# Performance work log

Hardware: AMD Instinct MI355X
Metric: run time of the kernel (lower is better)

## Reference

```python
import jax, jax.numpy as jnp
import numpy as np

NEG_SLOPE = 0.2  # PyG GATConv default leaky_relu slope


def _gat_layer(x, src, dst, n_nodes, W, a_src, a_dst, b, heads, out_ch):
    # x: [N, Fin] -> h: [N, H, C]
    h = (x @ W).reshape(n_nodes, heads, out_ch)
    alpha_s = jnp.einsum('nhc,hc->nh', h, a_src)  # [N, H]
    alpha_d = jnp.einsum('nhc,hc->nh', h, a_dst)  # [N, H]
    e = jax.nn.leaky_relu(alpha_s[src] + alpha_d[dst], NEG_SLOPE)  # [E, H]
    # segment softmax over edges grouped by destination node
    m = jax.ops.segment_max(e, dst, num_segments=n_nodes)          # [N, H]
    e = jnp.exp(e - m[dst])
    denom = jax.ops.segment_sum(e, dst, num_segments=n_nodes)      # [N, H]
    alpha = e / denom[dst]                                          # self-loops guarantee denom > 0
    msg = alpha[:, :, None] * h[src]                                # [E, H, C]
    out = jax.ops.segment_sum(msg, dst, num_segments=n_nodes)      # [N, H, C]
    return out.reshape(n_nodes, heads * out_ch) + b


def reference(x, edge_index, batch, W1, a_src1, a_dst1, b1, W2, a_src2, a_dst2, b2, fc_w, fc_b):
    n_nodes = x.shape[0]
    heads = a_src1.shape[0]
    # PyG GATConv adds self-loops by default
    loops = jnp.arange(n_nodes, dtype=edge_index.dtype)
    src = jnp.concatenate([edge_index[0], loops])
    dst = jnp.concatenate([edge_index[1], loops])

    h = _gat_layer(x, src, dst, n_nodes, W1, a_src1, a_dst1, b1, heads, 64)
    h = jax.nn.relu(h)  # dropout is identity in eval mode
    h = _gat_layer(h, src, dst, n_nodes, W2, a_src2, a_dst2, b2, heads, 16)
    h = jax.nn.relu(h)

    n_graphs = 64
    sums = jax.ops.segment_sum(h, batch, num_segments=n_graphs)                    # [G, 64]
    counts = jax.ops.segment_sum(jnp.ones((n_nodes,), h.dtype), batch, num_segments=n_graphs)
    pooled = sums / jnp.maximum(counts, 1.0)[:, None]                              # global_mean_pool
    return pooled @ fc_w + fc_b


def setup_inputs() -> dict:
    key = jax.random.key(0)
    ks = jax.random.split(key, 12)
    N, E, F_in, G = 50000, 800000, 128, 64
    H = 4
    x = jax.random.normal(ks[0], (N, F_in), jnp.float32)
    edge_index = jax.random.randint(ks[1], (2, E), 0, N, jnp.int32)
    batch = jnp.sort(jax.random.randint(ks[2], (N,), 0, G, jnp.int32))
    s1 = 1.0 / np.sqrt(F_in)
    s2 = 1.0 / np.sqrt(H * 64)
    s3 = 1.0 / np.sqrt(H * 16)
    return {
        'x': x,
        'edge_index': edge_index,
        'batch': batch,
        'W1': jax.random.normal(ks[3], (F_in, H * 64), jnp.float32) * s1,
        'a_src1': jax.random.normal(ks[4], (H, 64), jnp.float32) * s1,
        'a_dst1': jax.random.normal(ks[5], (H, 64), jnp.float32) * s1,
        'b1': jnp.zeros((H * 64,), jnp.float32),
        'W2': jax.random.normal(ks[6], (H * 64, H * 16), jnp.float32) * s2,
        'a_src2': jax.random.normal(ks[7], (H, 16), jnp.float32) * s2,
        'a_dst2': jax.random.normal(ks[8], (H, 16), jnp.float32) * s2,
        'b2': jnp.zeros((H * 16,), jnp.float32),
        'fc_w': jax.random.normal(ks[9], (H * 16, 32), jnp.float32) * s3,
        'fc_b': jnp.zeros((32,), jnp.float32),
    }
```

## Files before the change

### kernel.cpp

```cpp
#include <hip/hip_runtime.h>
#include <hip/hip_bf16.h>
#include <hip/hip_fp16.h>
#include <math.h>

#define HEADS 4
#define CAP 64

typedef _Float16 half8_t __attribute__((ext_vector_type(8)));
typedef float float4_t __attribute__((ext_vector_type(4)));


__global__ __launch_bounds__(256) void prep_k(int* cnt, unsigned short* slots, int N, int NB,
                                              const float* __restrict__ W1, _Float16* __restrict__ W1T,
                                              const float* __restrict__ W2, _Float16* __restrict__ W2T) {
    int bx = blockIdx.x;
    if (bx < NB) {
        int i = bx * 256 + threadIdx.x;
        if (i < N) {
            cnt[i] = 1;
            slots[(size_t)i * CAP] = (unsigned short)i;
        }
    } else if (bx < NB + 128) {
        int k = bx - NB;
        int n = threadIdx.x;
        W1T[n * 128 + k] = (_Float16)W1[k * 256 + n];
    } else {
        int n = bx - NB - 128;
        int k = threadIdx.x;
        W2T[n * 256 + k] = (_Float16)W2[k * 64 + n];
    }
}


__global__ __launch_bounds__(256) void fused_scatter_gemm1_k(
    const int* __restrict__ src, const int* __restrict__ dst,
    int* __restrict__ cnt, unsigned short* __restrict__ slots, int E, int SB,
    const float* __restrict__ A,
    const _Float16* __restrict__ BT,
    __half* __restrict__ hout,
    const float* __restrict__ avs,
    const float* __restrict__ avd,
    float* __restrict__ os,
    float* __restrict__ od, int M) {
    __shared__ _Float16 lds[4 * 16 * 72];

    if ((int)blockIdx.x < SB) {
        int T = SB * 256;
        int t0 = blockIdx.x * 256 + threadIdx.x;
        int d[8], s[8];
        #pragma unroll
        for (int k = 0; k < 8; k++) {
            int i = t0 + k * T;
            if (i < E) { d[k] = dst[i]; s[k] = src[i]; }
            else d[k] = -1;
        }
        int p[8];
        #pragma unroll
        for (int k = 0; k < 8; k++) {
            if (d[k] >= 0) p[k] = atomicAdd(&cnt[d[k]], 1);
        }
        #pragma unroll
        for (int k = 0; k < 8; k++) {
            if (d[k] >= 0 && p[k] < CAP)
                slots[(size_t)d[k] * CAP + p[k]] = (unsigned short)s[k];
        }
        return;
    }

    int bx = blockIdx.x - SB;
    int wave = threadIdx.x >> 6;
    int lane = threadIdx.x & 63;
    int q = lane >> 4;
    int c16 = lane & 15;
    int row0 = bx * 64 + wave * 16;

    half8_t a[4];
    int ar = row0 + c16;
    bool avalid = (ar < M);
    const float* ap = A + (size_t)ar * 128;
    #pragma unroll
    for (int ks = 0; ks < 4; ks++) {
        if (avalid) {
            float4 f0 = *(const float4*)(ap + ks * 32 + q * 8);
            float4 f1 = *(const float4*)(ap + ks * 32 + q * 8 + 4);
            half8_t h;
            h[0] = (_Float16)f0.x; h[1] = (_Float16)f0.y;
            h[2] = (_Float16)f0.z; h[3] = (_Float16)f0.w;
            h[4] = (_Float16)f1.x; h[5] = (_Float16)f1.y;
            h[6] = (_Float16)f1.z; h[7] = (_Float16)f1.w;
            a[ks] = h;
        } else {
            a[ks] = (half8_t)(_Float16)0.0f;
        }
    }

    float4_t acc[16];
    #pragma unroll
    for (int ct = 0; ct < 16; ct++) acc[ct] = (float4_t)0.f;

    #pragma unroll
    for (int ks = 0; ks < 4; ks++) {
        #pragma unroll
        for (int ct = 0; ct < 16; ct++) {
            half8_t b = *(const half8_t*)(BT + (size_t)(ct * 16 + c16) * 128 + ks * 32 + q * 8);
            acc[ct] = __builtin_amdgcn_mfma_f32_16x16x32_f16(a[ks], b, acc[ct], 0, 0, 0);
        }
    }

    float psh[4][4] = {}, pdh[4][4] = {};
    #pragma unroll
    for (int ct = 0; ct < 16; ct++) {
        int h = ct >> 2;
        int cih = (ct & 3) * 16 + c16;
        float as_v = avs[h * 64 + cih];
        float ad_v = avd[h * 64 + cih];
        #pragma unroll
        for (int r = 0; r < 4; r++) {
            psh[h][r] = fmaf(acc[ct][r], as_v, psh[h][r]);
            pdh[h][r] = fmaf(acc[ct][r], ad_v, pdh[h][r]);
        }
    }
    #pragma unroll
    for (int h = 0; h < 4; h++) {
        #pragma unroll
        for (int r = 0; r < 4; r++) {
            #pragma unroll
            for (int o = 8; o >= 1; o >>= 1) {
                psh[h][r] += __shfl_down(psh[h][r], o, 16);
                pdh[h][r] += __shfl_down(pdh[h][r], o, 16);
            }
        }
    }
    if (c16 == 0) {
        #pragma unroll
        for (int r = 0; r < 4; r++) {
            int gr = row0 + q * 4 + r;
            if (gr < M) {
                #pragma unroll
                for (int h = 0; h < 4; h++) {
                    os[(size_t)gr * HEADS + h] = psh[h][r];
                    od[(size_t)gr * HEADS + h] = pdh[h][r];
                }
            }
        }
    }

    _Float16* wl = lds + wave * (16 * 72);
    #pragma unroll
    for (int chunk = 0; chunk < 4; chunk++) {
        #pragma unroll
        for (int c4 = 0; c4 < 4; c4++) {
            int ct = chunk * 4 + c4;
            #pragma unroll
            for (int r = 0; r < 4; r++) {
                wl[(q * 4 + r) * 72 + c4 * 16 + c16] = (_Float16)acc[ct][r];
            }
        }
        __syncthreads();
        #pragma unroll
        for (int pass = 0; pass < 2; pass++) {
            int idx8 = pass * 64 + lane;
            int row = idx8 >> 3;
            int col8 = idx8 & 7;
            int gr = row0 + row;
            if (gr < M) {
                *(half8_t*)(hout + (size_t)gr * 256 + chunk * 64 + col8 * 8) =
                    *(const half8_t*)(wl + row * 72 + col8 * 8);
            }
        }
        __syncthreads();
    }
}


__global__ __launch_bounds__(256) void mfma_gemm2_k(
    const _Float16* __restrict__ Ah,
    const _Float16* __restrict__ BT,
    __half* __restrict__ hout,
    const float* __restrict__ avs,
    const float* __restrict__ avd,
    float* __restrict__ os,
    float* __restrict__ od, int M) {
    __shared__ _Float16 lds[4 * 16 * 64];
    int wave = threadIdx.x >> 6;
    int lane = threadIdx.x & 63;
    int q = lane >> 4;
    int c16 = lane & 15;
    int row0 = blockIdx.x * 64 + wave * 16;

    half8_t a[8];
    int ar = row0 + c16;
    bool avalid = (ar < M);
    const _Float16* ap = Ah + (size_t)ar * 256;
    #pragma unroll
    for (int ks = 0; ks < 8; ks++) {
        if (avalid) a[ks] = *(const half8_t*)(ap + ks * 32 + q * 8);
        else        a[ks] = (half8_t)(_Float16)0.0f;
    }

    float4_t acc[4];
    #pragma unroll
    for (int ct = 0; ct < 4; ct++) acc[ct] = (float4_t)0.f;

    #pragma unroll
    for (int ks = 0; ks < 8; ks++) {
        #pragma unroll
        for (int ct = 0; ct < 4; ct++) {
            half8_t b = *(const half8_t*)(BT + (size_t)(ct * 16 + c16) * 256 + ks * 32 + q * 8);
            acc[ct] = __builtin_amdgcn_mfma_f32_16x16x32_f16(a[ks], b, acc[ct], 0, 0, 0);
        }
    }

    float ps[4][4], pd[4][4];
    #pragma unroll
    for (int ct = 0; ct < 4; ct++) {
        float as_v = avs[ct * 16 + c16];
        float ad_v = avd[ct * 16 + c16];
        #pragma unroll
        for (int r = 0; r < 4; r++) {
            ps[ct][r] = acc[ct][r] * as_v;
            pd[ct][r] = acc[ct][r] * ad_v;
            #pragma unroll
            for (int o = 8; o >= 1; o >>= 1) {
                ps[ct][r] += __shfl_down(ps[ct][r], o, 16);
                pd[ct][r] += __shfl_down(pd[ct][r], o, 16);
            }
        }
    }
    if (c16 == 0) {
        #pragma unroll
        for (int r = 0; r < 4; r++) {
            int gr = row0 + q * 4 + r;
            if (gr < M) {
                #pragma unroll
                for (int ct = 0; ct < 4; ct++) {
                    os[(size_t)gr * HEADS + ct] = ps[ct][r];
                    od[(size_t)gr * HEADS + ct] = pd[ct][r];
                }
            }
        }
    }

    _Float16* wl = lds + wave * (16 * 64);
    #pragma unroll
    for (int ct = 0; ct < 4; ct++) {
        #pragma unroll
        for (int r = 0; r < 4; r++) {
            wl[(q * 4 + r) * 64 + ct * 16 + c16] = (_Float16)acc[ct][r];
        }
    }
    __syncthreads();
    #pragma unroll
    for (int pass = 0; pass < 2; pass++) {
        int idx8 = pass * 64 + lane;
        int row = idx8 >> 3;
        int col8 = idx8 & 7;
        int gr = row0 + row;
        if (gr < M) {
            *(half8_t*)(hout + (size_t)gr * 64 + col8 * 8) =
                *(const half8_t*)(wl + row * 64 + col8 * 8);
        }
    }
}


__global__ __launch_bounds__(256) void gat_agg64_f16_k(
    const __half* __restrict__ hsrc,
    const float* __restrict__ as,
    const float* __restrict__ ad,
    const int* __restrict__ cnt,
    const unsigned short* __restrict__ slots,
    const float* __restrict__ bias,
    __half* __restrict__ outh,
    int N) {
    int node = blockIdx.x * 4 + (threadIdx.x >> 6);
    if (node >= N) return;
    int l = threadIdx.x & 63;
    int h = l >> 4;
    int je = l & 15;
    int hb = h << 4;
    int deg = min(cnt[node], CAP);
    const unsigned short* sp = slots + (size_t)node * CAP;
    float adh = ad[(size_t)node * HEADS + h];
    float4 bv = *(const float4*)(bias + l * 4);

    int sv[4];
    float ev[4];
    #pragma unroll
    for (int k = 0; k < 4; k++) {
        int j = k * 16 + je;
        sv[k] = (j < deg) ? (int)sp[j] : 0;
    }
    #pragma unroll
    for (int k = 0; k < 4; k++) {
        int j = k * 16 + je;
        if (j < deg) {
            float a = as[(size_t)sv[k] * HEADS + h] + adh;
            ev[k] = (a > 0.f) ? a : 0.2f * a;
        } else {
            ev[k] = -INFINITY;
        }
    }
    float m = fmaxf(fmaxf(ev[0], ev[1]), fmaxf(ev[2], ev[3]));
    #pragma unroll
    for (int o = 8; o >= 1; o >>= 1) m = fmaxf(m, __shfl_xor(m, o));
    float pv[4];
    float den = 0.f;
    #pragma unroll
    for (int k = 0; k < 4; k++) {
        pv[k] = (k * 16 + je < deg) ? __expf(ev[k] - m) : 0.f;
        den += pv[k];
    }
    #pragma unroll
    for (int o = 8; o >= 1; o >>= 1) den += __shfl_xor(den, o);

    float4 acc = make_float4(0.f, 0.f, 0.f, 0.f);
    #pragma unroll
    for (int k = 0; k < 4; k++) {
        int base = k * 16;
        if (base >= deg) break;
        int cl = min(16, deg - base);
        #pragma unroll
        for (int half = 0; half < 2; half++) {
            int j0 = half * 8;
            if (j0 >= cl) break;
            float pj[8]; int sj[8];
            #pragma unroll
            for (int jj = 0; jj < 8; jj++) {
                pj[jj] = __shfl(pv[k], hb + j0 + jj);
                sj[jj] = __shfl(sv[k], hb + j0 + jj);
            }
            uint2 rv[8];
            #pragma unroll
            for (int jj = 0; jj < 8; jj++) {
                if (j0 + jj < cl) rv[jj] = *(const uint2*)(hsrc + (size_t)sj[jj] * 256 + l * 4);
            }
            #pragma unroll
            for (int jj = 0; jj < 8; jj++) {
                if (j0 + jj < cl) {
                    float2 a0 = __half22float2(*(__half2*)&rv[jj].x);
                    float2 b0 = __half22float2(*(__half2*)&rv[jj].y);
                    acc.x = fmaf(pj[jj], a0.x, acc.x); acc.y = fmaf(pj[jj], a0.y, acc.y);
                    acc.z = fmaf(pj[jj], b0.x, acc.z); acc.w = fmaf(pj[jj], b0.y, acc.w);
                }
            }
        }
    }

    float inv = 1.f / den;
    float rx = fmaxf(fmaf(acc.x, inv, bv.x), 0.f);
    float ry = fmaxf(fmaf(acc.y, inv, bv.y), 0.f);
    float rz = fmaxf(fmaf(acc.z, inv, bv.z), 0.f);
    float rw = fmaxf(fmaf(acc.w, inv, bv.w), 0.f);
    __half2* op = (__half2*)(outh + (size_t)node * 256 + l * 4);
    op[0] = __floats2half2_rn(rx, ry);
    op[1] = __floats2half2_rn(rz, rw);
}


__global__ __launch_bounds__(256) void gat_agg16_f16_k(
    const __half* __restrict__ hsrc,
    const float* __restrict__ as,
    const float* __restrict__ ad,
    const int* __restrict__ cnt,
    const unsigned short* __restrict__ slots,
    const float* __restrict__ bias,
    float* __restrict__ out, int N) {
    int node = blockIdx.x * 4 + (threadIdx.x >> 6);
    if (node >= N) return;
    int l = threadIdx.x & 63;
    int ha = l >> 4;
    int je = l & 15;
    int q = l & 15;
    int hh = q >> 2;
    int eg = l >> 4;
    int deg = min(cnt[node], CAP);
    const unsigned short* sp = slots + (size_t)node * CAP;
    float adh = ad[(size_t)node * HEADS + ha];
    float m = -INFINITY, den = 0.f;
    float4 acc = make_float4(0.f, 0.f, 0.f, 0.f);
    for (int base = 0; base < deg; base += 16) {
        int cl = min(16, deg - base);
        int s = 0;
        float e = -INFINITY;
        if (je < cl) {
            s = sp[base + je];
            float a = as[(size_t)s * HEADS + ha] + adh;
            e = (a > 0.f) ? a : 0.2f * a;
        }
        float cmax = e;
        #pragma unroll
        for (int o = 8; o >= 1; o >>= 1) cmax = fmaxf(cmax, __shfl_xor(cmax, o));
        float m_new = fmaxf(m, cmax);
        float p = (je < cl) ? __expf(e - m_new) : 0.f;
        float sum = p;
        #pragma unroll
        for (int o = 8; o >= 1; o >>= 1) sum += __shfl_xor(sum, o);
        float sc = __expf(m - m_new);
        den = den * sc + sum;
        m = m_new;
        float sch = __shfl(sc, hh << 4);
        acc.x *= sch; acc.y *= sch; acc.z *= sch; acc.w *= sch;

        int jbase = eg * 4;
        float pj[4]; int sj[4]; bool vj[4];
        #pragma unroll
        for (int jj = 0; jj < 4; jj++) {
            int j = jbase + jj;
            int jc = min(j, cl - 1);
            pj[jj] = __shfl(p, (hh << 4) + jc);
            sj[jj] = __shfl(s, (hh << 4) + jc);
            vj[jj] = (j < cl);
        }
        uint2 rv[4];
        #pragma unroll
        for (int jj = 0; jj < 4; jj++) {
            if (vj[jj]) rv[jj] = *(const uint2*)(hsrc + (size_t)sj[jj] * 64 + q * 4);
        }
        #pragma unroll
        for (int jj = 0; jj < 4; jj++) {
            if (vj[jj]) {
                float2 f0 = __half22float2(*(__half2*)&rv[jj].x);
                float2 f1 = __half22float2(*(__half2*)&rv[jj].y);
                acc.x = fmaf(pj[jj], f0.x, acc.x); acc.y = fmaf(pj[jj], f0.y, acc.y);
                acc.z = fmaf(pj[jj], f1.x, acc.z); acc.w = fmaf(pj[jj], f1.y, acc.w);
            }
        }
    }
    acc.x += __shfl_xor(acc.x, 16); acc.y += __shfl_xor(acc.y, 16);
    acc.z += __shfl_xor(acc.z, 16); acc.w += __shfl_xor(acc.w, 16);
    acc.x += __shfl_xor(acc.x, 32); acc.y += __shfl_xor(acc.y, 32);
    acc.z += __shfl_xor(acc.z, 32); acc.w += __shfl_xor(acc.w, 32);
    float denh = __shfl(den, hh << 4);
    if (eg == 0) {
        float inv = 1.f / denh;
        float4 bv = *(const float4*)(bias + q * 4);
        float4 r;
        r.x = fmaxf(fmaf(acc.x, inv, bv.x), 0.f);
        r.y = fmaxf(fmaf(acc.y, inv, bv.y), 0.f);
        r.z = fmaxf(fmaf(acc.z, inv, bv.z), 0.f);
        r.w = fmaxf(fmaf(acc.w, inv, bv.w), 0.f);
        *(float4*)(out + (size_t)node * 64 + q * 4) = r;
    }
}


__global__ __launch_bounds__(256) void bounds_zero_k(const int* __restrict__ batch, int N,
                                                     int* __restrict__ bstart,
                                                     float* __restrict__ sums) {
    int t = threadIdx.x;
    if (t <= 64) {
        int lo = 0, hi = N;
        while (lo < hi) {
            int mid = (lo + hi) >> 1;
            if (batch[mid] < t) lo = mid + 1; else hi = mid;
        }
        bstart[t] = lo;
    }
    for (int i = t; i < 64 * 64; i += 256) sums[i] = 0.f;
}

__global__ __launch_bounds__(256) void pool_sum_k(const float* __restrict__ g2,
                                                  const int* __restrict__ batch,
                                                  float* __restrict__ sums, int N) {
    int c = threadIdx.x & 63;
    int r = threadIdx.x >> 6;
    int base = blockIdx.x * 256;
    int lim = min(base + 256, N);
    float acc = 0.f;
    int cur = -1;
    for (int n = base + r; n < lim; n += 4) {
        int g = batch[n];
        if (g != cur) {
            if (cur >= 0) atomicAdd(&sums[cur * 64 + c], acc);
            acc = 0.f;
            cur = g;
        }
        acc += g2[(size_t)n * 64 + c];
    }
    if (cur >= 0) atomicAdd(&sums[cur * 64 + c], acc);
}

__global__ void fc_k(const float* __restrict__ sums, const int* __restrict__ bstart,
                     const float* __restrict__ w, const float* __restrict__ b,
                     float* __restrict__ out) {
    int g = blockIdx.x, o = threadIdx.x;
    float cnt_ = (float)max(bstart[g + 1] - bstart[g], 1);
    float inv = 1.f / cnt_;
    float acc = b[o];
    for (int k = 0; k < 64; k++) acc = fmaf(sums[g * 64 + k] * inv, w[k * 32 + o], acc);
    out[g * 32 + o] = acc;
}


static inline size_t align_up(size_t x, size_t a) { return (x + a - 1) & ~(a - 1); }

extern "C" void kernel_launch(void* const* d_in, const int* in_sizes, int n_in,
                              void* d_out, int out_size, void* d_ws, size_t ws_size,
                              hipStream_t stream) {
    const float* x      = (const float*)d_in[0];
    const int*   ei     = (const int*)d_in[1];
    const int*   batch  = (const int*)d_in[2];
    const float* W1     = (const float*)d_in[3];
    const float* a_src1 = (const float*)d_in[4];
    const float* a_dst1 = (const float*)d_in[5];
    const float* b1     = (const float*)d_in[6];
    const float* W2     = (const float*)d_in[7];
    const float* a_src2 = (const float*)d_in[8];
    const float* a_dst2 = (const float*)d_in[9];
    const float* b2     = (const float*)d_in[10];
    const float* fc_w   = (const float*)d_in[11];
    const float* fc_b   = (const float*)d_in[12];
    float* out = (float*)d_out;

    const int N = in_sizes[2];
    const int E = in_sizes[1] / 2;
    const int F_in = in_sizes[0] / N;
    const int D1 = HEADS * 64;
    const int D2 = HEADS * 16;

    const int* src = ei;
    const int* dst = ei + E;

    char* w = (char*)d_ws;
    size_t off = 0;
    auto alloc = [&](size_t bytes) {
        size_t p = off;
        off = align_up(off + bytes, 256);
        return (void*)(w + p);
    };
    int* cnt    = (int*)alloc((size_t)N * 4);
    unsigned short* slots = (unsigned short*)alloc((size_t)N * CAP * 2);
    int* bstart = (int*)alloc(65 * 4);
    float* pooled = (float*)alloc(64 * 64 * 4);
    float* as1  = (float*)alloc((size_t)N * HEADS * 4);
    float* ad1  = (float*)alloc((size_t)N * HEADS * 4);
    float* as2  = (float*)alloc((size_t)N * HEADS * 4);
    float* ad2  = (float*)alloc((size_t)N * HEADS * 4);
    __half* h1h = (__half*)alloc((size_t)N * D1 * 2);
    __half* g1h = (__half*)alloc((size_t)N * D1 * 2);
    __half* h2h = (__half*)alloc((size_t)N * D2 * 2);
    float* g2   = (float*)alloc((size_t)N * D2 * 4);
    _Float16* w1t = (_Float16*)alloc((size_t)F_in * D1 * 2);
    _Float16* w2t = (_Float16*)alloc((size_t)D1 * D2 * 2);

    const int NB = (N + 255) / 256;
    prep_k<<<NB + 128 + 64, 256, 0, stream>>>(cnt, slots, N, NB, W1, w1t, W2, w2t);

    const int SB = (E + 2047) / 2048;
    const int GB = (N + 63) / 64;
    fused_scatter_gemm1_k<<<SB + GB, 256, 0, stream>>>(
        src, dst, cnt, slots, E, SB,
        x, w1t, h1h, a_src1, a_dst1, as1, ad1, N);

    gat_agg64_f16_k<<<(N + 3) / 4, 256, 0, stream>>>(h1h, as1, ad1, cnt, slots, b1, g1h, N);

    mfma_gemm2_k<<<(N + 63) / 64, 256, 0, stream>>>((const _Float16*)g1h, w2t, h2h,
                                                    a_src2, a_dst2, as2, ad2, N);
    gat_agg16_f16_k<<<(N + 3) / 4, 256, 0, stream>>>(h2h, as2, ad2, cnt, slots, b2, g2, N);

    bounds_zero_k<<<1, 256, 0, stream>>>(batch, N, bstart, pooled);
    pool_sum_k<<<(N + 255) / 256, 256, 0, stream>>>(g2, batch, pooled, N);
    fc_k<<<64, 32, 0, stream>>>(pooled, bstart, fc_w, fc_b, out);
}
```

Baseline: 314.0 us.

## Replace global atomic edge scatter with chunked LDS byte-counter histogram and scan

Replaces the global-memory atomicAdd per edge on per-node counters with a two-pass scheme. Each of 128 edge chunks first builds a packed 8-bit per-node count histogram in LDS. A tiled column scan then turns those into per-chunk offsets, and a second pass places sources using LDS atomics. The bounds/zero kernel is also folded into prep_k. This aims to cut global atomic contention, but it adds a kernel launch, a 6.4MB count matrix and an extra read of dst. It also relies on 8-bit counters not overflowing: any carry out of a packed byte corrupts the neighbouring node's count, so high-degree nodes are a correctness risk.

```diff
diff --git a/kernel.cpp b/kernel.cpp
--- a/kernel.cpp
+++ b/kernel.cpp
@@ -5,36 +5,112 @@
 
 #define HEADS 4
 #define CAP 64
+#define NC 128
 
 typedef _Float16 half8_t __attribute__((ext_vector_type(8)));
 typedef float float4_t __attribute__((ext_vector_type(4)));
 
 
-__global__ __launch_bounds__(256) void prep_k(int* cnt, unsigned short* slots, int N, int NB,
+__global__ __launch_bounds__(256) void prep_k(unsigned short* slots, int N, int NB,
                                               const float* __restrict__ W1, _Float16* __restrict__ W1T,
-                                              const float* __restrict__ W2, _Float16* __restrict__ W2T) {
+                                              const float* __restrict__ W2, _Float16* __restrict__ W2T,
+                                              const int* __restrict__ dst, int E,
+                                              unsigned char* __restrict__ cnts8, int NS,
+                                              const int* __restrict__ batch,
+                                              int* __restrict__ bstart, float* __restrict__ sums) {
+    __shared__ unsigned int sh[12544];
     int bx = blockIdx.x;
-    if (bx < NB) {
-        int i = bx * 256 + threadIdx.x;
-        if (i < N) {
-            cnt[i] = 1;
-            slots[(size_t)i * CAP] = (unsigned short)i;
-        }
-    } else if (bx < NB + 128) {
-        int k = bx - NB;
+    if (bx < NC) {
+        int c = bx;
+        int nwt = NS >> 2;
+        for (int i = threadIdx.x; i < nwt; i += 256) sh[i] = 0u;
+        __syncthreads();
+        int epc = (E + NC - 1) / NC;
+        int lo = c * epc, hi = min(lo + epc, E);
+        for (int i = lo + threadIdx.x; i < hi; i += 256) {
+            int d = dst[i];
+            atomicAdd(&sh[d >> 2], 1u << ((d & 3) * 8));
+        }
+        __syncthreads();
+        unsigned int* row32 = (unsigned int*)(cnts8 + (size_t)c * NS);
+        for (int i = threadIdx.x; i < nwt; i += 256) row32[i] = sh[i];
+    } else if (bx < NC + NB) {
+        int i = (bx - NC) * 256 + threadIdx.x;
+        if (i < N) slots[(size_t)i * CAP] = (unsigned short)i;
+    } else if (bx < NC + NB + 128) {
+        int k = bx - NC - NB;
         int n = threadIdx.x;
         W1T[n * 128 + k] = (_Float16)W1[k * 256 + n];
-    } else {
-        int n = bx - NB - 128;
+    } else if (bx < NC + NB + 192) {
+        int n = bx - NC - NB - 128;
         int k = threadIdx.x;
         W2T[n * 256 + k] = (_Float16)W2[k * 64 + n];
-    }
-}
-
-
-__global__ __launch_bounds__(256) void fused_scatter_gemm1_k(
-    const int* __restrict__ src, const int* __restrict__ dst,
-    int* __restrict__ cnt, unsigned short* __restrict__ slots, int E, int SB,
+    } else {
+        int t = threadIdx.x;
+        if (t <= 64) {
+            int lo = 0, hi = N;
+            while (lo < hi) {
+                int mid = (lo + hi) >> 1;
+                if (batch[mid] < t) lo = mid + 1; else hi = mid;
+            }
+            bstart[t] = lo;
+        }
+        for (int i = t; i < 64 * 64; i += 256) sums[i] = 0.f;
+    }
+}
+
+
+__global__ __launch_bounds__(256) void scan_tile_k(unsigned char* __restrict__ cnts8,
+                                                   int NS, int N, int* __restrict__ cnt) {
+    __shared__ unsigned int tile[NC * 128];
+    int nwt = NS >> 2;
+    int wb = blockIdx.x * 128;
+    const unsigned int* g = (const unsigned int*)cnts8;
+    int rowstride = nwt;
+
+    for (int idx = threadIdx.x; idx < NC * 128; idx += 256) {
+        int c = idx >> 7;
+        int w = idx & 127;
+        int gw = wb + w;
+        if (gw < nwt) tile[c * 128 + w] = g[(size_t)c * rowstride + gw];
+    }
+    __syncthreads();
+
+    if (threadIdx.x < 128) {
+        int w = threadIdx.x;
+        int gw = wb + w;
+        if (gw < nwt) {
+            unsigned int a = 0x01010101u;
+            #pragma unroll 8
+            for (int c = 0; c < NC; c++) {
+                unsigned int v = tile[c * 128 + w];
+                tile[c * 128 + w] = a;
+                a += v;
+            }
+            int n0 = gw * 4;
+            #pragma unroll
+            for (int b = 0; b < 4; b++) {
+                int n = n0 + b;
+                if (n < N) cnt[n] = (int)((a >> (b * 8)) & 255u);
+            }
+        }
+    }
+    __syncthreads();
+
+    unsigned int* gm = (unsigned int*)cnts8;
+    for (int idx = threadIdx.x; idx < NC * 128; idx += 256) {
+        int c = idx >> 7;
+        int w = idx & 127;
+        int gw = wb + w;
+        if (gw < nwt) gm[(size_t)c * rowstride + gw] = tile[c * 128 + w];
+    }
+}
+
+
+__global__ __launch_bounds__(256) void fused_place_gemm1_k(
+    const int* __restrict__ src, const int* __restrict__ dst, int E,
+    unsigned char* __restrict__ offs8, int NS,
+    unsigned short* __restrict__ slots,
     const float* __restrict__ A,
     const _Float16* __restrict__ BT,
     __half* __restrict__ hout,
@@ -42,32 +118,28 @@
     const float* __restrict__ avd,
     float* __restrict__ os,
     float* __restrict__ od, int M) {
-    __shared__ _Float16 lds[4 * 16 * 72];
-
-    if ((int)blockIdx.x < SB) {
-        int T = SB * 256;
-        int t0 = blockIdx.x * 256 + threadIdx.x;
-        int d[8], s[8];
-        #pragma unroll
-        for (int k = 0; k < 8; k++) {
-            int i = t0 + k * T;
-            if (i < E) { d[k] = dst[i]; s[k] = src[i]; }
-            else d[k] = -1;
-        }
-        int p[8];
-        #pragma unroll
-        for (int k = 0; k < 8; k++) {
-            if (d[k] >= 0) p[k] = atomicAdd(&cnt[d[k]], 1);
-        }
-        #pragma unroll
-        for (int k = 0; k < 8; k++) {
-            if (d[k] >= 0 && p[k] < CAP)
-                slots[(size_t)d[k] * CAP + p[k]] = (unsigned short)s[k];
+    __shared__ unsigned int shmem[12544];
+
+    if ((int)blockIdx.x < NC) {
+        int c = blockIdx.x;
+        int nwt = NS >> 2;
+        const unsigned int* row = (const unsigned int*)(offs8 + (size_t)c * NS);
+        for (int i = threadIdx.x; i < nwt; i += 256) shmem[i] = row[i];
+        __syncthreads();
+        int epc = (E + NC - 1) / NC;
+        int lo = c * epc, hi = min(lo + epc, E);
+        for (int i = lo + threadIdx.x; i < hi; i += 256) {
+            int d = dst[i];
+            int s = src[i];
+            unsigned int old = atomicAdd(&shmem[d >> 2], 1u << ((d & 3) * 8));
+            int pos = (int)((old >> ((d & 3) * 8)) & 255u);
+            if (pos < CAP) slots[(size_t)d * CAP + pos] = (unsigned short)s;
         }
         return;
     }
 
-    int bx = blockIdx.x - SB;
+    _Float16* lds = (_Float16*)shmem;
+    int bx = blockIdx.x - NC;
     int wave = threadIdx.x >> 6;
     int lane = threadIdx.x & 63;
     int q = lane >> 4;
@@ -445,21 +517,6 @@
 }
 
 
-__global__ __launch_bounds__(256) void bounds_zero_k(const int* __restrict__ batch, int N,
-                                                     int* __restrict__ bstart,
-                                                     float* __restrict__ sums) {
-    int t = threadIdx.x;
-    if (t <= 64) {
-        int lo = 0, hi = N;
-        while (lo < hi) {
-            int mid = (lo + hi) >> 1;
-            if (batch[mid] < t) lo = mid + 1; else hi = mid;
-        }
-        bstart[t] = lo;
-    }
-    for (int i = t; i < 64 * 64; i += 256) sums[i] = 0.f;
-}
-
 __global__ __launch_bounds__(256) void pool_sum_k(const float* __restrict__ g2,
                                                   const int* __restrict__ batch,
                                                   float* __restrict__ sums, int N) {
@@ -518,6 +575,8 @@
     const int F_in = in_sizes[0] / N;
     const int D1 = HEADS * 64;
     const int D2 = HEADS * 16;
+    const int NS = (N + 3) & ~3;
+    const int nwt = NS >> 2;
 
     const int* src = ei;
     const int* dst = ei + E;
@@ -543,14 +602,17 @@
     float* g2   = (float*)alloc((size_t)N * D2 * 4);
     _Float16* w1t = (_Float16*)alloc((size_t)F_in * D1 * 2);
     _Float16* w2t = (_Float16*)alloc((size_t)D1 * D2 * 2);
+    unsigned char* cnts8 = (unsigned char*)alloc((size_t)NC * NS);
 
     const int NB = (N + 255) / 256;
-    prep_k<<<NB + 128 + 64, 256, 0, stream>>>(cnt, slots, N, NB, W1, w1t, W2, w2t);
-
-    const int SB = (E + 2047) / 2048;
+    prep_k<<<NC + NB + 192 + 1, 256, 0, stream>>>(slots, N, NB, W1, w1t, W2, w2t,
+                                                  dst, E, cnts8, NS, batch, bstart, pooled);
+
+    scan_tile_k<<<(nwt + 127) / 128, 256, 0, stream>>>(cnts8, NS, N, cnt);
+
     const int GB = (N + 63) / 64;
-    fused_scatter_gemm1_k<<<SB + GB, 256, 0, stream>>>(
-        src, dst, cnt, slots, E, SB,
+    fused_place_gemm1_k<<<NC + GB, 256, 0, stream>>>(
+        src, dst, E, cnts8, NS, slots,
         x, w1t, h1h, a_src1, a_dst1, as1, ad1, N);
 
     gat_agg64_f16_k<<<(N + 3) / 4, 256, 0, stream>>>(h1h, as1, ad1, cnt, slots, b1, g1h, N);
@@ -559,7 +621,6 @@
                                                     a_src2, a_dst2, as2, ad2, N);
     gat_agg16_f16_k<<<(N + 3) / 4, 256, 0, stream>>>(h2h, as2, ad2, cnt, slots, b2, g2, N);
 
-    bounds_zero_k<<<1, 256, 0, stream>>>(batch, N, bstart, pooled);
     pool_sum_k<<<(N + 255) / 256, 256, 0, stream>>>(g2, batch, pooled, N);
     fc_k<<<64, 32, 0, stream>>>(pooled, bstart, fc_w, fc_b, out);
 }
```

Result: no change. 315.7 us (+0.5%).

## Bucket edges by destination range in LDS counters and fuse pooling with FC

Applied to the files above, without the earlier changes.

The edge scatter no longer uses global atomics. Each of 256 blocks owns a contiguous range of destination nodes, scans the whole dst array, and keeps per-node counters in LDS, writing the final counts to global memory once at the end. The separate cnt/slots init, the bounds/zero kernel and the atomic pool_sum plus fc kernels are merged into prep_k and a single per-graph poolfc_k that reduces with no atomics. The trade is that every scatter block reads all of dst (about 256 times the dst traffic, mostly absorbed by L2), in exchange for removing contended global atomics and several kernel launches.

```diff
diff --git a/kernel.cpp b/kernel.cpp
--- a/kernel.cpp
+++ b/kernel.cpp
@@ -5,36 +5,42 @@
 
 #define HEADS 4
 #define CAP 64
+#define SBL 256
 
 typedef _Float16 half8_t __attribute__((ext_vector_type(8)));
 typedef float float4_t __attribute__((ext_vector_type(4)));
 
 
-__global__ __launch_bounds__(256) void prep_k(int* cnt, unsigned short* slots, int N, int NB,
-                                              const float* __restrict__ W1, _Float16* __restrict__ W1T,
-                                              const float* __restrict__ W2, _Float16* __restrict__ W2T) {
+__global__ __launch_bounds__(256) void prep_k(const float* __restrict__ W1, _Float16* __restrict__ W1T,
+                                              const float* __restrict__ W2, _Float16* __restrict__ W2T,
+                                              const int* __restrict__ batch, int N,
+                                              int* __restrict__ bstart) {
     int bx = blockIdx.x;
-    if (bx < NB) {
-        int i = bx * 256 + threadIdx.x;
-        if (i < N) {
-            cnt[i] = 1;
-            slots[(size_t)i * CAP] = (unsigned short)i;
-        }
-    } else if (bx < NB + 128) {
-        int k = bx - NB;
+    if (bx < 128) {
+        int k = bx;
         int n = threadIdx.x;
         W1T[n * 128 + k] = (_Float16)W1[k * 256 + n];
-    } else {
-        int n = bx - NB - 128;
+    } else if (bx < 192) {
+        int n = bx - 128;
         int k = threadIdx.x;
         W2T[n * 256 + k] = (_Float16)W2[k * 64 + n];
+    } else {
+        int t = threadIdx.x;
+        if (t <= 64) {
+            int lo = 0, hi = N;
+            while (lo < hi) {
+                int mid = (lo + hi) >> 1;
+                if (batch[mid] < t) lo = mid + 1; else hi = mid;
+            }
+            bstart[t] = lo;
+        }
     }
 }
 
 
 __global__ __launch_bounds__(256) void fused_scatter_gemm1_k(
-    const int* __restrict__ src, const int* __restrict__ dst,
-    int* __restrict__ cnt, unsigned short* __restrict__ slots, int E, int SB,
+    const int* __restrict__ src, const int* __restrict__ dst, int E,
+    int* __restrict__ cnt, unsigned short* __restrict__ slots, int Nn,
     const float* __restrict__ A,
     const _Float16* __restrict__ BT,
     __half* __restrict__ hout,
@@ -42,32 +48,71 @@
     const float* __restrict__ avd,
     float* __restrict__ os,
     float* __restrict__ od, int M) {
+    __shared__ int lc[512];
     __shared__ _Float16 lds[4 * 16 * 72];
 
-    if ((int)blockIdx.x < SB) {
-        int T = SB * 256;
-        int t0 = blockIdx.x * 256 + threadIdx.x;
-        int d[8], s[8];
-        #pragma unroll
-        for (int k = 0; k < 8; k++) {
-            int i = t0 + k * T;
-            if (i < E) { d[k] = dst[i]; s[k] = src[i]; }
-            else d[k] = -1;
-        }
-        int p[8];
-        #pragma unroll
-        for (int k = 0; k < 8; k++) {
-            if (d[k] >= 0) p[k] = atomicAdd(&cnt[d[k]], 1);
-        }
-        #pragma unroll
-        for (int k = 0; k < 8; k++) {
-            if (d[k] >= 0 && p[k] < CAP)
-                slots[(size_t)d[k] * CAP + p[k]] = (unsigned short)s[k];
-        }
+    if ((int)blockIdx.x < SBL) {
+        int b = blockIdx.x;
+        int NR = (Nn + SBL - 1) / SBL;
+        int lo = b * NR, hi = min(lo + NR, Nn);
+        int nloc = hi - lo;
+        int t = threadIdx.x;
+        for (int j = t; j < nloc; j += 256) {
+            lc[j] = 1;
+            slots[(size_t)(lo + j) * CAP] = (unsigned short)(lo + j);
+        }
+        __syncthreads();
+
+        const int4* dst4 = (const int4*)dst;
+        int nq = E >> 2;
+        int base = 0;
+        for (; base + 1024 <= nq; base += 1024) {
+            int4 v[4];
+            #pragma unroll
+            for (int k = 0; k < 4; k++) v[k] = dst4[base + t + k * 256];
+            #pragma unroll
+            for (int k = 0; k < 4; k++) {
+                int i0 = (base + t + k * 256) * 4;
+                int dd[4] = { v[k].x, v[k].y, v[k].z, v[k].w };
+                #pragma unroll
+                for (int e = 0; e < 4; e++) {
+                    int d = dd[e];
+                    if (d >= lo && d < hi) {
+                        int s = src[i0 + e];
+                        int pos = atomicAdd(&lc[d - lo], 1);
+                        if (pos < CAP) slots[(size_t)d * CAP + pos] = (unsigned short)s;
+                    }
+                }
+            }
+        }
+        for (int i4 = base + t; i4 < nq; i4 += 256) {
+            int4 v = dst4[i4];
+            int i0 = i4 * 4;
+            int dd[4] = { v.x, v.y, v.z, v.w };
+            #pragma unroll
+            for (int e = 0; e < 4; e++) {
+                int d = dd[e];
+                if (d >= lo && d < hi) {
+                    int s = src[i0 + e];
+                    int pos = atomicAdd(&lc[d - lo], 1);
+                    if (pos < CAP) slots[(size_t)d * CAP + pos] = (unsigned short)s;
+                }
+            }
+        }
+        for (int i = (nq << 2) + t; i < E; i += 256) {
+            int d = dst[i];
+            if (d >= lo && d < hi) {
+                int s = src[i];
+                int pos = atomicAdd(&lc[d - lo], 1);
+                if (pos < CAP) slots[(size_t)d * CAP + pos] = (unsigned short)s;
+            }
+        }
+        __syncthreads();
+        for (int j = t; j < nloc; j += 256) cnt[lo + j] = lc[j];
         return;
     }
 
-    int bx = blockIdx.x - SB;
+    int bx = blockIdx.x - SBL;
     int wave = threadIdx.x >> 6;
     int lane = threadIdx.x & 63;
     int q = lane >> 4;
@@ -445,51 +490,34 @@
 }
 
 
-__global__ __launch_bounds__(256) void bounds_zero_k(const int* __restrict__ batch, int N,
-                                                     int* __restrict__ bstart,
-                                                     float* __restrict__ sums) {
-    int t = threadIdx.x;
-    if (t <= 64) {
-        int lo = 0, hi = N;
-        while (lo < hi) {
-            int mid = (lo + hi) >> 1;
-            if (batch[mid] < t) lo = mid + 1; else hi = mid;
-        }
-        bstart[t] = lo;
-    }
-    for (int i = t; i < 64 * 64; i += 256) sums[i] = 0.f;
-}
-
-__global__ __launch_bounds__(256) void pool_sum_k(const float* __restrict__ g2,
-                                                  const int* __restrict__ batch,
-                                                  float* __restrict__ sums, int N) {
+__global__ __launch_bounds__(256) void poolfc_k(const float* __restrict__ g2,
+                                                const int* __restrict__ bstart,
+                                                const float* __restrict__ w,
+                                                const float* __restrict__ b,
+                                                float* __restrict__ out) {
+    __shared__ float red[4][64];
+    __shared__ float pooled[64];
+    int g = blockIdx.x;
+    int lo = bstart[g], hi = bstart[g + 1];
     int c = threadIdx.x & 63;
     int r = threadIdx.x >> 6;
-    int base = blockIdx.x * 256;
-    int lim = min(base + 256, N);
     float acc = 0.f;
-    int cur = -1;
-    for (int n = base + r; n < lim; n += 4) {
-        int g = batch[n];
-        if (g != cur) {
-            if (cur >= 0) atomicAdd(&sums[cur * 64 + c], acc);
-            acc = 0.f;
-            cur = g;
-        }
-        acc += g2[(size_t)n * 64 + c];
-    }
-    if (cur >= 0) atomicAdd(&sums[cur * 64 + c], acc);
-}
-
-__global__ void fc_k(const float* __restrict__ sums, const int* __restrict__ bstart,
-                     const float* __restrict__ w, const float* __restrict__ b,
-                     float* __restrict__ out) {
-    int g = blockIdx.x, o = threadIdx.x;
-    float cnt_ = (float)max(bstart[g + 1] - bstart[g], 1);
-    float inv = 1.f / cnt_;
-    float acc = b[o];
-    for (int k = 0; k < 64; k++) acc = fmaf(sums[g * 64 + k] * inv, w[k * 32 + o], acc);
-    out[g * 32 + o] = acc;
+    for (int n = lo + r; n < hi; n += 4) acc += g2[(size_t)n * 64 + c];
+    red[r][c] = acc;
+    __syncthreads();
+    if (threadIdx.x < 64) {
+        float inv = 1.f / (float)max(hi - lo, 1);
+        pooled[threadIdx.x] = (red[0][threadIdx.x] + red[1][threadIdx.x] +
+                               red[2][threadIdx.x] + red[3][threadIdx.x]) * inv;
+    }
+    __syncthreads();
+    if (threadIdx.x < 32) {
+        int o = threadIdx.x;
+        float a = b[o];
+        #pragma unroll 8
+        for (int k = 0; k < 64; k++) a = fmaf(pooled[k], w[k * 32 + o], a);
+        out[g * 32 + o] = a;
+    }
 }
 
 
@@ -532,7 +560,6 @@
     int* cnt    = (int*)alloc((size_t)N * 4);
     unsigned short* slots = (unsigned short*)alloc((size_t)N * CAP * 2);
     int* bstart = (int*)alloc(65 * 4);
-    float* pooled = (float*)alloc(64 * 64 * 4);
     float* as1  = (float*)alloc((size_t)N * HEADS * 4);
     float* ad1  = (float*)alloc((size_t)N * HEADS * 4);
     float* as2  = (float*)alloc((size_t)N * HEADS * 4);
@@ -544,13 +571,11 @@
     _Float16* w1t = (_Float16*)alloc((size_t)F_in * D1 * 2);
     _Float16* w2t = (_Float16*)alloc((size_t)D1 * D2 * 2);
 
-    const int NB = (N + 255) / 256;
-    prep_k<<<NB + 128 + 64, 256, 0, stream>>>(cnt, slots, N, NB, W1, w1t, W2, w2t);
-
-    const int SB = (E + 2047) / 2048;
+    prep_k<<<193, 256, 0, stream>>>(W1, w1t, W2, w2t, batch, N, bstart);
+
     const int GB = (N + 63) / 64;
-    fused_scatter_gemm1_k<<<SB + GB, 256, 0, stream>>>(
-        src, dst, cnt, slots, E, SB,
+    fused_scatter_gemm1_k<<<SBL + GB, 256, 0, stream>>>(
+        src, dst, E, cnt, slots, N,
         x, w1t, h1h, a_src1, a_dst1, as1, ad1, N);
 
     gat_agg64_f16_k<<<(N + 3) / 4, 256, 0, stream>>>(h1h, as1, ad1, cnt, slots, b1, g1h, N);
@@ -559,7 +584,5 @@
                                                     a_src2, a_dst2, as2, ad2, N);
     gat_agg16_f16_k<<<(N + 3) / 4, 256, 0, stream>>>(h2h, as2, ad2, cnt, slots, b2, g2, N);
 
-    bounds_zero_k<<<1, 256, 0, stream>>>(batch, N, bstart, pooled);
-    pool_sum_k<<<(N + 255) / 256, 256, 0, stream>>>(g2, batch, pooled, N);
-    fc_k<<<64, 32, 0, stream>>>(pooled, bstart, fc_w, fc_b, out);
-}
+    poolfc_k<<<64, 256, 0, stream>>>(g2, bstart, fc_w, fc_b, out);
+}
```

Result: slower. 554.9 us (+76.7%).

## Fuse pooling and FC into one kernel, fold bounds search into prep, widen gather batch

Applied to the files above, without the earlier changes.

Computes the graph boundary binary search inside the prep kernel, removing the standalone bounds/zero launch. Replaces the atomic pool_sum and fc kernels with a single per-graph kernel that reduces that graph's contiguous rows, averages them and applies the FC layer, saving two launches and the atomics. Also widens the layer-1 aggregation gather from batches of 8 to 16 neighbour loads in flight. The per-graph pool kernel runs only 64 blocks, each reading about 780 rows serially, so it may have less parallelism than the old atomic version.

```diff
diff --git a/kernel.cpp b/kernel.cpp
--- a/kernel.cpp
+++ b/kernel.cpp
@@ -12,7 +12,8 @@
 
 __global__ __launch_bounds__(256) void prep_k(int* cnt, unsigned short* slots, int N, int NB,
                                               const float* __restrict__ W1, _Float16* __restrict__ W1T,
-                                              const float* __restrict__ W2, _Float16* __restrict__ W2T) {
+                                              const float* __restrict__ W2, _Float16* __restrict__ W2T,
+                                              const int* __restrict__ batch, int* __restrict__ bstart) {
     int bx = blockIdx.x;
     if (bx < NB) {
         int i = bx * 256 + threadIdx.x;
@@ -24,10 +25,20 @@
         int k = bx - NB;
         int n = threadIdx.x;
         W1T[n * 128 + k] = (_Float16)W1[k * 256 + n];
-    } else {
+    } else if (bx < NB + 192) {
         int n = bx - NB - 128;
         int k = threadIdx.x;
         W2T[n * 256 + k] = (_Float16)W2[k * 64 + n];
+    } else {
+        int t = threadIdx.x;
+        if (t <= 64) {
+            int lo = 0, hi = N;
+            while (lo < hi) {
+                int mid = (lo + hi) >> 1;
+                if (batch[mid] < t) lo = mid + 1; else hi = mid;
+            }
+            bstart[t] = lo;
+        }
     }
 }
 
@@ -320,29 +331,22 @@
         int base = k * 16;
         if (base >= deg) break;
         int cl = min(16, deg - base);
-        #pragma unroll
-        for (int half = 0; half < 2; half++) {
-            int j0 = half * 8;
-            if (j0 >= cl) break;
-            float pj[8]; int sj[8];
-            #pragma unroll
-            for (int jj = 0; jj < 8; jj++) {
-                pj[jj] = __shfl(pv[k], hb + j0 + jj);
-                sj[jj] = __shfl(sv[k], hb + j0 + jj);
-            }
-            uint2 rv[8];
-            #pragma unroll
-            for (int jj = 0; jj < 8; jj++) {
-                if (j0 + jj < cl) rv[jj] = *(const uint2*)(hsrc + (size_t)sj[jj] * 256 + l * 4);
-            }
-            #pragma unroll
-            for (int jj = 0; jj < 8; jj++) {
-                if (j0 + jj < cl) {
-                    float2 a0 = __half22float2(*(__half2*)&rv[jj].x);
-                    float2 b0 = __half22float2(*(__half2*)&rv[jj].y);
-                    acc.x = fmaf(pj[jj], a0.x, acc.x); acc.y = fmaf(pj[jj], a0.y, acc.y);
-                    acc.z = fmaf(pj[jj], b0.x, acc.z); acc.w = fmaf(pj[jj], b0.y, acc.w);
-                }
+        int sj[16];
+        #pragma unroll
+        for (int jj = 0; jj < 16; jj++) sj[jj] = __shfl(sv[k], hb + jj);
+        uint2 rv[16];
+        #pragma unroll
+        for (int jj = 0; jj < 16; jj++) {
+            if (jj < cl) rv[jj] = *(const uint2*)(hsrc + (size_t)sj[jj] * 256 + l * 4);
+        }
+        #pragma unroll
+        for (int jj = 0; jj < 16; jj++) {
+            if (jj < cl) {
+                float pj = __shfl(pv[k], hb + jj);
+                float2 a0 = __half22float2(*(__half2*)&rv[jj].x);
+                float2 b0 = __half22float2(*(__half2*)&rv[jj].y);
+                acc.x = fmaf(pj, a0.x, acc.x); acc.y = fmaf(pj, a0.y, acc.y);
+                acc.z = fmaf(pj, b0.x, acc.z); acc.w = fmaf(pj, b0.y, acc.w);
             }
         }
     }
@@ -445,51 +449,34 @@
 }
 
 
-__global__ __launch_bounds__(256) void bounds_zero_k(const int* __restrict__ batch, int N,
-                                                     int* __restrict__ bstart,
-                                                     float* __restrict__ sums) {
-    int t = threadIdx.x;
-    if (t <= 64) {
-        int lo = 0, hi = N;
-        while (lo < hi) {
-            int mid = (lo + hi) >> 1;
-            if (batch[mid] < t) lo = mid + 1; else hi = mid;
-        }
-        bstart[t] = lo;
-    }
-    for (int i = t; i < 64 * 64; i += 256) sums[i] = 0.f;
-}
-
-__global__ __launch_bounds__(256) void pool_sum_k(const float* __restrict__ g2,
-                                                  const int* __restrict__ batch,
-                                                  float* __restrict__ sums, int N) {
+__global__ __launch_bounds__(256) void poolfc_k(const float* __restrict__ g2,
+                                                const int* __restrict__ bstart,
+                                                const float* __restrict__ w,
+                                                const float* __restrict__ b,
+                                                float* __restrict__ out) {
+    __shared__ float red[4][64];
+    __shared__ float pooled[64];
+    int g = blockIdx.x;
+    int lo = bstart[g], hi = bstart[g + 1];
     int c = threadIdx.x & 63;
     int r = threadIdx.x >> 6;
-    int base = blockIdx.x * 256;
-    int lim = min(base + 256, N);
     float acc = 0.f;
-    int cur = -1;
-    for (int n = base + r; n < lim; n += 4) {
-        int g = batch[n];
-        if (g != cur) {
-            if (cur >= 0) atomicAdd(&sums[cur * 64 + c], acc);
-            acc = 0.f;
-            cur = g;
-        }
-        acc += g2[(size_t)n * 64 + c];
-    }
-    if (cur >= 0) atomicAdd(&sums[cur * 64 + c], acc);
-}
-
-__global__ void fc_k(const float* __restrict__ sums, const int* __restrict__ bstart,
-                     const float* __restrict__ w, const float* __restrict__ b,
-                     float* __restrict__ out) {
-    int g = blockIdx.x, o = threadIdx.x;
-    float cnt_ = (float)max(bstart[g + 1] - bstart[g], 1);
-    float inv = 1.f / cnt_;
-    float acc = b[o];
-    for (int k = 0; k < 64; k++) acc = fmaf(sums[g * 64 + k] * inv, w[k * 32 + o], acc);
-    out[g * 32 + o] = acc;
+    for (int n = lo + r; n < hi; n += 4) acc += g2[(size_t)n * 64 + c];
+    red[r][c] = acc;
+    __syncthreads();
+    if (threadIdx.x < 64) {
+        float inv = 1.f / (float)max(hi - lo, 1);
+        pooled[threadIdx.x] = (red[0][threadIdx.x] + red[1][threadIdx.x] +
+                               red[2][threadIdx.x] + red[3][threadIdx.x]) * inv;
+    }
+    __syncthreads();
+    if (threadIdx.x < 32) {
+        int o = threadIdx.x;
+        float a = b[o];
+        #pragma unroll 8
+        for (int k = 0; k < 64; k++) a = fmaf(pooled[k], w[k * 32 + o], a);
+        out[g * 32 + o] = a;
+    }
 }
 
 
@@ -532,7 +519,6 @@
     int* cnt    = (int*)alloc((size_t)N * 4);
     unsigned short* slots = (unsigned short*)alloc((size_t)N * CAP * 2);
     int* bstart = (int*)alloc(65 * 4);
-    float* pooled = (float*)alloc(64 * 64 * 4);
     float* as1  = (float*)alloc((size_t)N * HEADS * 4);
     float* ad1  = (float*)alloc((size_t)N * HEADS * 4);
     float* as2  = (float*)alloc((size_t)N * HEADS * 4);
@@ -545,7 +531,8 @@
     _Float16* w2t = (_Float16*)alloc((size_t)D1 * D2 * 2);
 
     const int NB = (N + 255) / 256;
-    prep_k<<<NB + 128 + 64, 256, 0, stream>>>(cnt, slots, N, NB, W1, w1t, W2, w2t);
+    prep_k<<<NB + 192 + 1, 256, 0, stream>>>(cnt, slots, N, NB, W1, w1t, W2, w2t,
+                                             batch, bstart);
 
     const int SB = (E + 2047) / 2048;
     const int GB = (N + 63) / 64;
@@ -559,7 +546,5 @@
                                                     a_src2, a_dst2, as2, ad2, N);
     gat_agg16_f16_k<<<(N + 3) / 4, 256, 0, stream>>>(h2h, as2, ad2, cnt, slots, b2, g2, N);
 
-    bounds_zero_k<<<1, 256, 0, stream>>>(batch, N, bstart, pooled);
-    pool_sum_k<<<(N + 255) / 256, 256, 0, stream>>>(g2, batch, pooled, N);
-    fc_k<<<64, 32, 0, stream>>>(pooled, bstart, fc_w, fc_b, out);
-}
+    poolfc_k<<<64, 256, 0, stream>>>(g2, bstart, fc_w, fc_b, out);
+}
```

Result: slower. 344.6 us (+9.7%).
